# Kernel tuning notes

Measured on AMD Instinct MI355X. Metric: run time of the kernel, lower is better.

Reference implementation:

```python
import jax, jax.numpy as jnp
import numpy as np

N_NODES = 100000
N_EDGES = 1600000
N_GRAPHS = 64
IN_FEATS = 86  # 10 + |NodeTypes|(3) + |Devices|(5) + 2*2 + 2*32
GCN_H = 64
FC_H = 32
BN_EPS = 1e-5


def setup_inputs() -> dict:
    key = jax.random.key(0)
    ks = jax.random.split(key, 10)
    x = jax.random.normal(ks[0], (N_NODES, IN_FEATS), dtype=jnp.float32)
    edge_src = jax.random.randint(ks[1], (N_EDGES,), 0, N_NODES, dtype=jnp.int32)
    edge_dst = jax.random.randint(ks[2], (N_EDGES,), 0, N_NODES, dtype=jnp.int32)
    graph_ids = jnp.sort(jax.random.randint(ks[3], (N_NODES,), 0, N_GRAPHS, dtype=jnp.int32))
    bn_gamma = jnp.ones((IN_FEATS,), dtype=jnp.float32)
    bn_beta = jnp.zeros((IN_FEATS,), dtype=jnp.float32)
    W1 = jax.random.normal(ks[4], (IN_FEATS, GCN_H), dtype=jnp.float32) * 0.1
    b1 = jnp.zeros((GCN_H,), dtype=jnp.float32)
    W2 = jax.random.normal(ks[5], (GCN_H, GCN_H), dtype=jnp.float32) * 0.1
    b2 = jnp.zeros((GCN_H,), dtype=jnp.float32)
    fc1_w = jax.random.normal(ks[6], (GCN_H, FC_H), dtype=jnp.float32) * 0.1
    fc1_b = jnp.zeros((FC_H,), dtype=jnp.float32)
    fc2_w = jax.random.normal(ks[7], (FC_H, 1), dtype=jnp.float32) * 0.1
    fc2_b = jnp.zeros((1,), dtype=jnp.float32)
    return {"x": x, "edge_src": edge_src, "edge_dst": edge_dst,
            "graph_ids": graph_ids, "num_graphs": N_GRAPHS,
            "bn_gamma": bn_gamma, "bn_beta": bn_beta,
            "W1": W1, "b1": b1, "W2": W2, "b2": b2,
            "fc1_w": fc1_w, "fc1_b": fc1_b, "fc2_w": fc2_w, "fc2_b": fc2_b}


def _gcn_layer(h, edge_src, edge_dst, W, b):
    # DGL copy_src + mean reduce: each node's h is overwritten by the mean of
    # its in-neighbors' h; zero-in-degree nodes keep their old h (UDF reduce
    # is only applied to nodes with non-empty mailboxes).
    n = h.shape[0]
    msg_sum = jax.ops.segment_sum(h[edge_src], edge_dst, num_segments=n)  # [N, d]
    deg = jax.ops.segment_sum(jnp.ones_like(edge_dst, dtype=h.dtype), edge_dst, num_segments=n)
    agg = jnp.where(deg[:, None] > 0, msg_sum / jnp.maximum(deg, 1.0)[:, None], h)
    return jax.nn.relu(agg @ W + b)


def reference(x, edge_src, edge_dst, graph_ids, num_graphs,
              bn_gamma, bn_beta, W1, b1, W2, b2, fc1_w, fc1_b, fc2_w, fc2_b):
    # BatchNorm1d in training mode: batch stats, biased variance.
    mean = jnp.mean(x, axis=0)
    var = jnp.mean(jnp.square(x - mean), axis=0)
    h = (x - mean) * jax.lax.rsqrt(var + BN_EPS) * bn_gamma + bn_beta
    # Two GCN layers (mean message passing + linear + ReLU).
    h = _gcn_layer(h, edge_src, edge_dst, W1, b1)
    h = _gcn_layer(h, edge_src, edge_dst, W2, b2)
    # dgl.mean_nodes over the batched graph: per-graph mean of node features.
    g_sum = jax.ops.segment_sum(h, graph_ids, num_segments=num_graphs)  # [B, d]
    g_cnt = jax.ops.segment_sum(jnp.ones_like(graph_ids, dtype=h.dtype), graph_ids, num_segments=num_graphs)
    hg = g_sum / jnp.maximum(g_cnt, 1.0)[:, None]
    # FC head (no activation between the two linears, matching the source).
    hg = hg @ fc1_w + fc1_b
    hg = hg @ fc2_w + fc2_b
    return jax.nn.sigmoid(hg).squeeze()
```

## Files before the change

kernel.cpp:

```cpp
#include <hip/hip_runtime.h>

#define N_NODES 100000
#define N_EDGES 1600000
#define N_GRAPHS_C 64
#define IN_F 86
#define H 64
#define N_BKT 391
#define SC_EPT 8
#define SC_TILE 2048
#define SC_GRID 782
#define NW_POOL 2048
typedef unsigned short ushort;

__device__ inline float bf2f(ushort u) { return __uint_as_float(((unsigned)u) << 16); }
__device__ inline ushort f2bf(float f) {
    unsigned x = __float_as_uint(f);
    return (ushort)((x + 0x7fffu + ((x >> 16) & 1u)) >> 16);
}

__global__ void bn_stats_k(const float* __restrict__ x,
                           float* __restrict__ bnsum, float* __restrict__ bnsq) {
    __shared__ float s1[IN_F], s2[IN_F];
    int tid = threadIdx.x;
    if (tid < IN_F) { s1[tid] = 0.f; s2[tid] = 0.f; }
    __syncthreads();
    const int T = 430 * 256;
    int t = blockIdx.x * 256 + tid;
    float sum = 0.f, sq = 0.f;
    for (int idx = t; idx < N_NODES * IN_F; idx += T) {
        float v = x[idx];
        sum += v; sq += v * v;
    }
    int f = t % IN_F;
    atomicAdd(&s1[f], sum);
    atomicAdd(&s2[f], sq);
    __syncthreads();
    if (tid < IN_F) {
        atomicAdd(&bnsum[tid], s1[tid]);
        atomicAdd(&bnsq[tid], s2[tid]);
    }
}

__global__ void prep_k(const float* __restrict__ bnsum, const float* __restrict__ bnsq,
                       const float* __restrict__ gamma, const float* __restrict__ beta,
                       const float* __restrict__ W1, const float* __restrict__ b1,
                       float* __restrict__ W1p, float* __restrict__ c1) {
    __shared__ float scale[IN_F], shift[IN_F];
    int t = threadIdx.x;
    if (t < IN_F) {
        float mean = bnsum[t] * (1.0f / N_NODES);
        float var  = bnsq[t] * (1.0f / N_NODES) - mean * mean;
        float sc = gamma[t] * rsqrtf(var + 1e-5f);
        scale[t] = sc;
        shift[t] = beta[t] - mean * sc;
    }
    __syncthreads();
    for (int idx = t; idx < IN_F * H; idx += blockDim.x) {
        int i = idx / H;
        W1p[idx] = scale[i] * W1[idx];
    }
    if (t < H) {
        float acc = b1[t];
        for (int i = 0; i < IN_F; i++) acc += shift[i] * W1[i * H + t];
        c1[t] = acc;
    }
}

__global__ void bucket_count_k(const int* __restrict__ dst, int* __restrict__ bcnt) {
    __shared__ int hist[N_BKT];
    int tid = threadIdx.x;
    for (int i = tid; i < N_BKT; i += 256) hist[i] = 0;
    __syncthreads();
    int e0 = blockIdx.x * SC_TILE;
#pragma unroll
    for (int i = 0; i < SC_EPT; i++) {
        int e = e0 + i * 256 + tid;
        if (e < N_EDGES) atomicAdd(&hist[dst[e] >> 8], 1);
    }
    __syncthreads();
    for (int i = tid; i < N_BKT; i += 256) atomicAdd(&bcnt[i], hist[i]);
}

__global__ void bucket_scan_k(const int* __restrict__ bcnt, int* __restrict__ bstart,
                              int* __restrict__ gcursor) {
    __shared__ int tmp[512];
    int t = threadIdx.x;
    int v = (t < N_BKT) ? bcnt[t] : 0;
    tmp[t] = v;
    __syncthreads();
    for (int off = 1; off < 512; off <<= 1) {
        int a = (t >= off) ? tmp[t - off] : 0;
        __syncthreads();
        tmp[t] += a;
        __syncthreads();
    }
    if (t < N_BKT) { bstart[t] = tmp[t] - v; gcursor[t] = tmp[t] - v; }
    if (t == N_BKT - 1) bstart[N_BKT] = tmp[t];
}

__global__ void bucket_scatter_k(const int* __restrict__ src, const int* __restrict__ dst,
                                 int* __restrict__ gcursor, unsigned* __restrict__ ebkt) {
    __shared__ int hist[N_BKT];
    __shared__ int base[N_BKT];
    int tid = threadIdx.x;
    for (int i = tid; i < N_BKT; i += 256) hist[i] = 0;
    __syncthreads();
    int e0 = blockIdx.x * SC_TILE;
    unsigned pk[SC_EPT];
    int bk[SC_EPT], lo[SC_EPT];
#pragma unroll
    for (int i = 0; i < SC_EPT; i++) {
        int e = e0 + i * 256 + tid;
        if (e < N_EDGES) {
            int d = dst[e];
            pk[i] = ((unsigned)src[e] << 8) | (unsigned)(d & 255);
            bk[i] = d >> 8;
            lo[i] = atomicAdd(&hist[bk[i]], 1);
        }
    }
    __syncthreads();
    for (int i = tid; i < N_BKT; i += 256) base[i] = atomicAdd(&gcursor[i], hist[i]);
    __syncthreads();
#pragma unroll
    for (int i = 0; i < SC_EPT; i++) {
        int e = e0 + i * 256 + tid;
        if (e < N_EDGES) ebkt[base[bk[i]] + lo[i]] = pk[i];
    }
}

__global__ void bucket_fill_k(const unsigned* __restrict__ ebkt, const int* __restrict__ bstart,
                              int* __restrict__ rs, int* __restrict__ csr) {
    __shared__ int deg[256];
    __shared__ int scn[256];
    __shared__ int cur[256];
    int b = blockIdx.x;
    int tid = threadIdx.x;
    int e0 = bstart[b], e1 = bstart[b + 1];
    deg[tid] = 0;
    __syncthreads();
    for (int e = e0 + tid; e < e1; e += 256) atomicAdd(&deg[ebkt[e] & 255u], 1);
    __syncthreads();
    scn[tid] = deg[tid];
    __syncthreads();
    for (int off = 1; off < 256; off <<= 1) {
        int a = (tid >= off) ? scn[tid - off] : 0;
        __syncthreads();
        scn[tid] += a;
        __syncthreads();
    }
    int node = (b << 8) + tid;
    if (node < N_NODES) rs[node] = e0 + scn[tid];
    cur[tid] = e0 + scn[tid] - deg[tid];
    __syncthreads();
    for (int e = e0 + tid; e < e1; e += 256) {
        unsigned p = ebkt[e];
        int pos = atomicAdd(&cur[p & 255u], 1);
        csr[pos] = (int)(p >> 8);
    }
}

template <int K>
__global__ __launch_bounds__(256) void gemm_t(const float* __restrict__ X,
                                              const float* __restrict__ W,
                                              const float* __restrict__ bias,
                                              ushort* __restrict__ Y, int N) {
    __shared__ __align__(16) float Xl[64][K + 1];
    __shared__ __align__(16) float Wl[K][64];
    int tid = threadIdx.x;
    int row0 = blockIdx.x * 64;
    for (int i = tid; i < K * 64; i += 256) Wl[i / 64][i % 64] = W[i];
    for (int i = tid; i < 64 * K; i += 256) {
        int r = i / K, c = i % K;
        Xl[r][c] = (row0 + r < N) ? X[(size_t)(row0 + r) * K + c] : 0.f;
    }
    __syncthreads();
    int cg = tid & 15, rg = tid >> 4;
    float4 b4 = *(const float4*)&bias[cg * 4];
    float acc[4][4];
    for (int i = 0; i < 4; i++) { acc[i][0] = b4.x; acc[i][1] = b4.y; acc[i][2] = b4.z; acc[i][3] = b4.w; }
    for (int k = 0; k < K; k++) {
        float4 w = *(const float4*)&Wl[k][cg * 4];
        float x0 = Xl[rg * 4 + 0][k];
        float x1 = Xl[rg * 4 + 1][k];
        float x2 = Xl[rg * 4 + 2][k];
        float x3 = Xl[rg * 4 + 3][k];
        acc[0][0] += x0 * w.x; acc[0][1] += x0 * w.y; acc[0][2] += x0 * w.z; acc[0][3] += x0 * w.w;
        acc[1][0] += x1 * w.x; acc[1][1] += x1 * w.y; acc[1][2] += x1 * w.z; acc[1][3] += x1 * w.w;
        acc[2][0] += x2 * w.x; acc[2][1] += x2 * w.y; acc[2][2] += x2 * w.z; acc[2][3] += x2 * w.w;
        acc[3][0] += x3 * w.x; acc[3][1] += x3 * w.y; acc[3][2] += x3 * w.z; acc[3][3] += x3 * w.w;
    }
    for (int i = 0; i < 4; i++) {
        int gr = row0 + rg * 4 + i;
        if (gr < N) {
            ushort4 o;
            o.x = f2bf(acc[i][0]); o.y = f2bf(acc[i][1]);
            o.z = f2bf(acc[i][2]); o.w = f2bf(acc[i][3]);
            *(ushort4*)&Y[(size_t)gr * 64 + cg * 4] = o;
        }
    }
}

__global__ void gather_f32_k(const ushort* __restrict__ g, const int* __restrict__ rs,
                             const int* __restrict__ csr, float* __restrict__ out) {
    int lane = threadIdx.x & 63;
    int n = blockIdx.x * (blockDim.x >> 6) + (threadIdx.x >> 6);
    if (n >= N_NODES) return;
    int start = (n == 0) ? 0 : rs[n - 1];
    int end = rs[n];
    float a0 = 0.f, a1 = 0.f, a2 = 0.f, a3 = 0.f;
    for (int j0 = start; j0 < end; j0 += 64) {
        int cnt = min(64, end - j0);
        int myidx = (lane < cnt) ? csr[j0 + lane] : 0;
        int j = 0;
        for (; j + 3 < cnt; j += 4) {
            int s0 = __shfl(myidx, j, 64);
            int s1 = __shfl(myidx, j + 1, 64);
            int s2 = __shfl(myidx, j + 2, 64);
            int s3 = __shfl(myidx, j + 3, 64);
            a0 += bf2f(g[(size_t)s0 * H + lane]);
            a1 += bf2f(g[(size_t)s1 * H + lane]);
            a2 += bf2f(g[(size_t)s2 * H + lane]);
            a3 += bf2f(g[(size_t)s3 * H + lane]);
        }
        for (; j < cnt; j++) {
            int s = __shfl(myidx, j, 64);
            a0 += bf2f(g[(size_t)s * H + lane]);
        }
    }
    int d = end - start;
    float acc = (a0 + a1) + (a2 + a3);
    float val = (d > 0) ? acc / (float)d : bf2f(g[(size_t)n * H + lane]);
    out[(size_t)n * H + lane] = fmaxf(val, 0.f);
}

__global__ void gather_bf16_k(const ushort* __restrict__ g, const int* __restrict__ rs,
                              const int* __restrict__ csr, ushort* __restrict__ out) {
    int lane = threadIdx.x & 63;
    int n = blockIdx.x * (blockDim.x >> 6) + (threadIdx.x >> 6);
    if (n >= N_NODES) return;
    int start = (n == 0) ? 0 : rs[n - 1];
    int end = rs[n];
    float a0 = 0.f, a1 = 0.f, a2 = 0.f, a3 = 0.f;
    for (int j0 = start; j0 < end; j0 += 64) {
        int cnt = min(64, end - j0);
        int myidx = (lane < cnt) ? csr[j0 + lane] : 0;
        int j = 0;
        for (; j + 3 < cnt; j += 4) {
            int s0 = __shfl(myidx, j, 64);
            int s1 = __shfl(myidx, j + 1, 64);
            int s2 = __shfl(myidx, j + 2, 64);
            int s3 = __shfl(myidx, j + 3, 64);
            a0 += bf2f(g[(size_t)s0 * H + lane]);
            a1 += bf2f(g[(size_t)s1 * H + lane]);
            a2 += bf2f(g[(size_t)s2 * H + lane]);
            a3 += bf2f(g[(size_t)s3 * H + lane]);
        }
        for (; j < cnt; j++) {
            int s = __shfl(myidx, j, 64);
            a0 += bf2f(g[(size_t)s * H + lane]);
        }
    }
    int d = end - start;
    float acc = (a0 + a1) + (a2 + a3);
    float val = (d > 0) ? acc / (float)d : bf2f(g[(size_t)n * H + lane]);
    out[(size_t)n * H + lane] = f2bf(fmaxf(val, 0.f));
}

__global__ void pool_k(const ushort* __restrict__ h, const int* __restrict__ gid,
                       float* __restrict__ gsum, int* __restrict__ gcnt) {
    int lane = threadIdx.x & 63;
    int wpb = blockDim.x >> 6;
    int gw = blockIdx.x * wpb + (threadIdx.x >> 6);
    const int chunk = (N_NODES + NW_POOL - 1) / NW_POOL;
    int n0 = gw * chunk;
    if (n0 >= N_NODES) return;
    int n1 = min(n0 + chunk, N_NODES);
    float acc = 0.f;
    int cur = gid[n0], cnt = 0;
    for (int n = n0; n < n1; n++) {
        int g = gid[n];
        if (g != cur) {
            atomicAdd(&gsum[cur * H + lane], acc);
            if (lane == 0) atomicAdd(&gcnt[cur], cnt);
            cur = g; acc = 0.f; cnt = 0;
        }
        acc += bf2f(h[(size_t)n * H + lane]);
        cnt++;
    }
    atomicAdd(&gsum[cur * H + lane], acc);
    if (lane == 0) atomicAdd(&gcnt[cur], cnt);
}

__global__ void head_k(const float* __restrict__ gsum, const int* __restrict__ gcnt,
                       const float* __restrict__ fc1w, const float* __restrict__ fc1b,
                       const float* __restrict__ fc2w, const float* __restrict__ fc2b,
                       float* __restrict__ out) {
    __shared__ float w1[H * 32];
    __shared__ float w2[32], bb1[32];
    int b = threadIdx.x;
    for (int i = b; i < H * 32; i += 64) w1[i] = fc1w[i];
    if (b < 32) { w2[b] = fc2w[b]; bb1[b] = fc1b[b]; }
    __syncthreads();
    if (b >= N_GRAPHS_C) return;
    float hg[H];
    float inv = 1.0f / fmaxf((float)gcnt[b], 1.0f);
    for (int k = 0; k < H; k++) hg[k] = gsum[b * H + k] * inv;
    float z = fc2b[0];
    for (int j = 0; j < 32; j++) {
        float t = bb1[j];
        for (int k = 0; k < H; k++) t += hg[k] * w1[k * 32 + j];
        z += t * w2[j];
    }
    out[b] = 1.0f / (1.0f + expf(-z));
}

extern "C" void kernel_launch(void* const* d_in, const int* in_sizes, int n_in,
                              void* d_out, int out_size, void* d_ws, size_t ws_size,
                              hipStream_t stream) {
    const float* x        = (const float*)d_in[0];
    const int*   edge_src = (const int*)d_in[1];
    const int*   edge_dst = (const int*)d_in[2];
    const int*   gid      = (const int*)d_in[3];
    const float* bn_gamma = (const float*)d_in[5];
    const float* bn_beta  = (const float*)d_in[6];
    const float* W1       = (const float*)d_in[7];
    const float* b1       = (const float*)d_in[8];
    const float* W2       = (const float*)d_in[9];
    const float* b2       = (const float*)d_in[10];
    const float* fc1w     = (const float*)d_in[11];
    const float* fc1b     = (const float*)d_in[12];
    const float* fc2w     = (const float*)d_in[13];
    const float* fc2b     = (const float*)d_in[14];
    float* out = (float*)d_out;

    char* ws = (char*)d_ws;
    size_t off = 0;
    auto alloc = [&](size_t bytes) { void* p = ws + off; off += (bytes + 255) & ~(size_t)255; return p; };
    float* bnsum    = (float*)alloc(IN_F * sizeof(float) * 2);
    float* bnsq     = bnsum + IN_F;
    float* W1p      = (float*)alloc(IN_F * H * sizeof(float));
    float* c1       = (float*)alloc(H * sizeof(float));
    float* gsum     = (float*)alloc(N_GRAPHS_C * H * sizeof(float) + N_GRAPHS_C * sizeof(int));
    int*   gcnt     = (int*)(gsum + N_GRAPHS_C * H);
    int*   bcnt     = (int*)alloc(N_BKT * sizeof(int));
    int*   bstart   = (int*)alloc((N_BKT + 1) * sizeof(int));
    int*   gcursor  = (int*)alloc(N_BKT * sizeof(int));
    int*   rs       = (int*)alloc(N_NODES * sizeof(int));
    int*   csr      = (int*)alloc((size_t)N_EDGES * sizeof(int));
    ushort* gbuf    = (ushort*)alloc((size_t)N_NODES * H * sizeof(ushort));
    float* agg      = (float*)alloc((size_t)N_NODES * H * sizeof(float));
    unsigned* ebkt = (unsigned*)gbuf;
    ushort* h2 = (ushort*)agg;

    hipMemsetAsync(bnsum, 0, IN_F * sizeof(float) * 2, stream);
    hipMemsetAsync(bcnt, 0, N_BKT * sizeof(int), stream);
    hipMemsetAsync(gsum, 0, N_GRAPHS_C * H * sizeof(float) + N_GRAPHS_C * sizeof(int), stream);

    bucket_count_k<<<SC_GRID, 256, 0, stream>>>(edge_dst, bcnt);
    bucket_scan_k<<<1, 512, 0, stream>>>(bcnt, bstart, gcursor);
    bucket_scatter_k<<<SC_GRID, 256, 0, stream>>>(edge_src, edge_dst, gcursor, ebkt);
    bucket_fill_k<<<N_BKT, 256, 0, stream>>>(ebkt, bstart, rs, csr);

    bn_stats_k<<<430, 256, 0, stream>>>(x, bnsum, bnsq);
    prep_k<<<1, 256, 0, stream>>>(bnsum, bnsq, bn_gamma, bn_beta, W1, b1, W1p, c1);

    gemm_t<IN_F><<<(N_NODES + 63) / 64, 256, 0, stream>>>(x, W1p, c1, gbuf, N_NODES);
    gather_f32_k<<<(N_NODES + 3) / 4, 256, 0, stream>>>(gbuf, rs, csr, agg);

    gemm_t<H><<<(N_NODES + 63) / 64, 256, 0, stream>>>(agg, W2, b2, gbuf, N_NODES);
    gather_bf16_k<<<(N_NODES + 3) / 4, 256, 0, stream>>>(gbuf, rs, csr, h2);

    pool_k<<<NW_POOL / 4, 256, 0, stream>>>(h2, gid, gsum, gcnt);
    head_k<<<1, 64, 0, stream>>>(gsum, gcnt, fc1w, fc1b, fc2w, fc2b, out);
}
```

Baseline: 428.2 us.

## Fuse BN stats with bucket count, scan with prep, pool into gather; bf16 h1

Merges the BN statistics pass with the edge bucket histogram, and the bucket scan with the weight-prep kernel, which removes two launches. The layer-1 output is now stored as bf16 instead of fp32, with a bf16-input GEMM for layer 2, which halves that intermediate's traffic. The second gather now does graph pooling directly through per-node atomics. The gather inner loop is unrolled to 8 independent accumulators, and the three memsets are combined into one. Per-node atomics on 64 graph rows can cause heavy contention, and the bf16 intermediate adds rounding error.

New measurement: 1.079 ms. 2.52x slower.

```diff
diff --git a/kernel.cpp b/kernel.cpp
--- a/kernel.cpp
+++ b/kernel.cpp
@@ -9,7 +9,7 @@
 #define SC_EPT 8
 #define SC_TILE 2048
 #define SC_GRID 782
-#define NW_POOL 2048
+#define BC_GRID 860
 typedef unsigned short ushort;
 
 __device__ inline float bf2f(ushort u) { return __uint_as_float(((unsigned)u) << 16); }
@@ -18,13 +18,24 @@
     return (ushort)((x + 0x7fffu + ((x >> 16) & 1u)) >> 16);
 }
 
-__global__ void bn_stats_k(const float* __restrict__ x,
-                           float* __restrict__ bnsum, float* __restrict__ bnsq) {
+__global__ void bn_count_k(const float* __restrict__ x, const int* __restrict__ dst,
+                           float* __restrict__ bnsum, float* __restrict__ bnsq,
+                           int* __restrict__ bcnt) {
     __shared__ float s1[IN_F], s2[IN_F];
+    __shared__ int hist[N_BKT];
     int tid = threadIdx.x;
     if (tid < IN_F) { s1[tid] = 0.f; s2[tid] = 0.f; }
-    __syncthreads();
-    const int T = 430 * 256;
+    for (int i = tid; i < N_BKT; i += 256) hist[i] = 0;
+    __syncthreads();
+    if (blockIdx.x < SC_GRID) {
+        int e0 = blockIdx.x * SC_TILE;
+#pragma unroll
+        for (int i = 0; i < SC_EPT; i++) {
+            int e = e0 + i * 256 + tid;
+            if (e < N_EDGES) atomicAdd(&hist[dst[e] >> 8], 1);
+        }
+    }
+    const int T = BC_GRID * 256;
     int t = blockIdx.x * 256 + tid;
     float sum = 0.f, sq = 0.f;
     for (int idx = t; idx < N_NODES * IN_F; idx += T) {
@@ -39,14 +50,30 @@
         atomicAdd(&bnsum[tid], s1[tid]);
         atomicAdd(&bnsq[tid], s2[tid]);
     }
-}
-
-__global__ void prep_k(const float* __restrict__ bnsum, const float* __restrict__ bnsq,
-                       const float* __restrict__ gamma, const float* __restrict__ beta,
-                       const float* __restrict__ W1, const float* __restrict__ b1,
-                       float* __restrict__ W1p, float* __restrict__ c1) {
+    if (blockIdx.x < SC_GRID)
+        for (int i = tid; i < N_BKT; i += 256) atomicAdd(&bcnt[i], hist[i]);
+}
+
+__global__ void scanprep_k(const int* __restrict__ bcnt, int* __restrict__ bstart,
+                           int* __restrict__ gcursor,
+                           const float* __restrict__ bnsum, const float* __restrict__ bnsq,
+                           const float* __restrict__ gamma, const float* __restrict__ beta,
+                           const float* __restrict__ W1, const float* __restrict__ b1,
+                           float* __restrict__ W1p, float* __restrict__ c1) {
+    __shared__ int tmp[512];
     __shared__ float scale[IN_F], shift[IN_F];
     int t = threadIdx.x;
+    int v = (t < N_BKT) ? bcnt[t] : 0;
+    tmp[t] = v;
+    __syncthreads();
+    for (int off = 1; off < 512; off <<= 1) {
+        int a = (t >= off) ? tmp[t - off] : 0;
+        __syncthreads();
+        tmp[t] += a;
+        __syncthreads();
+    }
+    if (t < N_BKT) { bstart[t] = tmp[t] - v; gcursor[t] = tmp[t] - v; }
+    if (t == N_BKT - 1) bstart[N_BKT] = tmp[t];
     if (t < IN_F) {
         float mean = bnsum[t] * (1.0f / N_NODES);
         float var  = bnsq[t] * (1.0f / N_NODES) - mean * mean;
@@ -55,47 +82,12 @@
         shift[t] = beta[t] - mean * sc;
     }
     __syncthreads();
-    for (int idx = t; idx < IN_F * H; idx += blockDim.x) {
-        int i = idx / H;
-        W1p[idx] = scale[i] * W1[idx];
-    }
+    for (int idx = t; idx < IN_F * H; idx += 512) W1p[idx] = scale[idx / H] * W1[idx];
     if (t < H) {
         float acc = b1[t];
         for (int i = 0; i < IN_F; i++) acc += shift[i] * W1[i * H + t];
         c1[t] = acc;
     }
-}
-
-__global__ void bucket_count_k(const int* __restrict__ dst, int* __restrict__ bcnt) {
-    __shared__ int hist[N_BKT];
-    int tid = threadIdx.x;
-    for (int i = tid; i < N_BKT; i += 256) hist[i] = 0;
-    __syncthreads();
-    int e0 = blockIdx.x * SC_TILE;
-#pragma unroll
-    for (int i = 0; i < SC_EPT; i++) {
-        int e = e0 + i * 256 + tid;
-        if (e < N_EDGES) atomicAdd(&hist[dst[e] >> 8], 1);
-    }
-    __syncthreads();
-    for (int i = tid; i < N_BKT; i += 256) atomicAdd(&bcnt[i], hist[i]);
-}
-
-__global__ void bucket_scan_k(const int* __restrict__ bcnt, int* __restrict__ bstart,
-                              int* __restrict__ gcursor) {
-    __shared__ int tmp[512];
-    int t = threadIdx.x;
-    int v = (t < N_BKT) ? bcnt[t] : 0;
-    tmp[t] = v;
-    __syncthreads();
-    for (int off = 1; off < 512; off <<= 1) {
-        int a = (t >= off) ? tmp[t - off] : 0;
-        __syncthreads();
-        tmp[t] += a;
-        __syncthreads();
-    }
-    if (t < N_BKT) { bstart[t] = tmp[t] - v; gcursor[t] = tmp[t] - v; }
-    if (t == N_BKT - 1) bstart[N_BKT] = tmp[t];
 }
 
 __global__ void bucket_scatter_k(const int* __restrict__ src, const int* __restrict__ dst,
@@ -159,13 +151,13 @@
     }
 }
 
-template <int K>
-__global__ __launch_bounds__(256) void gemm_t(const float* __restrict__ X,
-                                              const float* __restrict__ W,
-                                              const float* __restrict__ bias,
-                                              ushort* __restrict__ Y, int N) {
-    __shared__ __align__(16) float Xl[64][K + 1];
-    __shared__ __align__(16) float Wl[K][64];
+__global__ __launch_bounds__(256) void gemm_f32_k(const float* __restrict__ X,
+                                                  const float* __restrict__ W,
+                                                  const float* __restrict__ bias,
+                                                  ushort* __restrict__ Y, int N) {
+    const int K = IN_F;
+    __shared__ __align__(16) float Xl[64][IN_F + 1];
+    __shared__ __align__(16) float Wl[IN_F][64];
     int tid = threadIdx.x;
     int row0 = blockIdx.x * 64;
     for (int i = tid; i < K * 64; i += 256) Wl[i / 64][i % 64] = W[i];
@@ -200,18 +192,80 @@
     }
 }
 
-__global__ void gather_f32_k(const ushort* __restrict__ g, const int* __restrict__ rs,
-                             const int* __restrict__ csr, float* __restrict__ out) {
-    int lane = threadIdx.x & 63;
-    int n = blockIdx.x * (blockDim.x >> 6) + (threadIdx.x >> 6);
-    if (n >= N_NODES) return;
-    int start = (n == 0) ? 0 : rs[n - 1];
-    int end = rs[n];
+__global__ __launch_bounds__(256) void gemm_bf16_k(const ushort* __restrict__ X,
+                                                   const float* __restrict__ W,
+                                                   const float* __restrict__ bias,
+                                                   ushort* __restrict__ Y, int N) {
+    const int K = H;
+    __shared__ __align__(16) float Xl[64][H + 1];
+    __shared__ __align__(16) float Wl[H][64];
+    int tid = threadIdx.x;
+    int row0 = blockIdx.x * 64;
+    for (int i = tid; i < K * 64; i += 256) Wl[i / 64][i % 64] = W[i];
+    for (int i = tid; i < 64 * 16; i += 256) {
+        int r = i >> 4, c4 = (i & 15) * 4;
+        if (row0 + r < N) {
+            ushort4 u = *(const ushort4*)&X[(size_t)(row0 + r) * K + c4];
+            Xl[r][c4 + 0] = bf2f(u.x); Xl[r][c4 + 1] = bf2f(u.y);
+            Xl[r][c4 + 2] = bf2f(u.z); Xl[r][c4 + 3] = bf2f(u.w);
+        } else {
+            Xl[r][c4 + 0] = 0.f; Xl[r][c4 + 1] = 0.f;
+            Xl[r][c4 + 2] = 0.f; Xl[r][c4 + 3] = 0.f;
+        }
+    }
+    __syncthreads();
+    int cg = tid & 15, rg = tid >> 4;
+    float4 b4 = *(const float4*)&bias[cg * 4];
+    float acc[4][4];
+    for (int i = 0; i < 4; i++) { acc[i][0] = b4.x; acc[i][1] = b4.y; acc[i][2] = b4.z; acc[i][3] = b4.w; }
+    for (int k = 0; k < K; k++) {
+        float4 w = *(const float4*)&Wl[k][cg * 4];
+        float x0 = Xl[rg * 4 + 0][k];
+        float x1 = Xl[rg * 4 + 1][k];
+        float x2 = Xl[rg * 4 + 2][k];
+        float x3 = Xl[rg * 4 + 3][k];
+        acc[0][0] += x0 * w.x; acc[0][1] += x0 * w.y; acc[0][2] += x0 * w.z; acc[0][3] += x0 * w.w;
+        acc[1][0] += x1 * w.x; acc[1][1] += x1 * w.y; acc[1][2] += x1 * w.z; acc[1][3] += x1 * w.w;
+        acc[2][0] += x2 * w.x; acc[2][1] += x2 * w.y; acc[2][2] += x2 * w.z; acc[2][3] += x2 * w.w;
+        acc[3][0] += x3 * w.x; acc[3][1] += x3 * w.y; acc[3][2] += x3 * w.z; acc[3][3] += x3 * w.w;
+    }
+    for (int i = 0; i < 4; i++) {
+        int gr = row0 + rg * 4 + i;
+        if (gr < N) {
+            ushort4 o;
+            o.x = f2bf(acc[i][0]); o.y = f2bf(acc[i][1]);
+            o.z = f2bf(acc[i][2]); o.w = f2bf(acc[i][3]);
+            *(ushort4*)&Y[(size_t)gr * 64 + cg * 4] = o;
+        }
+    }
+}
+
+__device__ inline float gather_row(const ushort* __restrict__ g, const int* __restrict__ csr,
+                                   int start, int end, int lane) {
     float a0 = 0.f, a1 = 0.f, a2 = 0.f, a3 = 0.f;
+    float a4 = 0.f, a5 = 0.f, a6 = 0.f, a7 = 0.f;
     for (int j0 = start; j0 < end; j0 += 64) {
         int cnt = min(64, end - j0);
         int myidx = (lane < cnt) ? csr[j0 + lane] : 0;
         int j = 0;
+        for (; j + 7 < cnt; j += 8) {
+            int s0 = __shfl(myidx, j, 64);
+            int s1 = __shfl(myidx, j + 1, 64);
+            int s2 = __shfl(myidx, j + 2, 64);
+            int s3 = __shfl(myidx, j + 3, 64);
+            int s4 = __shfl(myidx, j + 4, 64);
+            int s5 = __shfl(myidx, j + 5, 64);
+            int s6 = __shfl(myidx, j + 6, 64);
+            int s7 = __shfl(myidx, j + 7, 64);
+            a0 += bf2f(g[(size_t)s0 * H + lane]);
+            a1 += bf2f(g[(size_t)s1 * H + lane]);
+            a2 += bf2f(g[(size_t)s2 * H + lane]);
+            a3 += bf2f(g[(size_t)s3 * H + lane]);
+            a4 += bf2f(g[(size_t)s4 * H + lane]);
+            a5 += bf2f(g[(size_t)s5 * H + lane]);
+            a6 += bf2f(g[(size_t)s6 * H + lane]);
+            a7 += bf2f(g[(size_t)s7 * H + lane]);
+        }
         for (; j + 3 < cnt; j += 4) {
             int s0 = __shfl(myidx, j, 64);
             int s1 = __shfl(myidx, j + 1, 64);
@@ -227,68 +281,37 @@
             a0 += bf2f(g[(size_t)s * H + lane]);
         }
     }
-    int d = end - start;
-    float acc = (a0 + a1) + (a2 + a3);
-    float val = (d > 0) ? acc / (float)d : bf2f(g[(size_t)n * H + lane]);
-    out[(size_t)n * H + lane] = fmaxf(val, 0.f);
-}
-
-__global__ void gather_bf16_k(const ushort* __restrict__ g, const int* __restrict__ rs,
-                              const int* __restrict__ csr, ushort* __restrict__ out) {
+    return ((a0 + a1) + (a2 + a3)) + ((a4 + a5) + (a6 + a7));
+}
+
+__global__ void gather1_k(const ushort* __restrict__ g, const int* __restrict__ rs,
+                          const int* __restrict__ csr, ushort* __restrict__ out) {
     int lane = threadIdx.x & 63;
-    int n = blockIdx.x * (blockDim.x >> 6) + (threadIdx.x >> 6);
+    int n = blockIdx.x * 4 + (threadIdx.x >> 6);
     if (n >= N_NODES) return;
     int start = (n == 0) ? 0 : rs[n - 1];
     int end = rs[n];
-    float a0 = 0.f, a1 = 0.f, a2 = 0.f, a3 = 0.f;
-    for (int j0 = start; j0 < end; j0 += 64) {
-        int cnt = min(64, end - j0);
-        int myidx = (lane < cnt) ? csr[j0 + lane] : 0;
-        int j = 0;
-        for (; j + 3 < cnt; j += 4) {
-            int s0 = __shfl(myidx, j, 64);
-            int s1 = __shfl(myidx, j + 1, 64);
-            int s2 = __shfl(myidx, j + 2, 64);
-            int s3 = __shfl(myidx, j + 3, 64);
-            a0 += bf2f(g[(size_t)s0 * H + lane]);
-            a1 += bf2f(g[(size_t)s1 * H + lane]);
-            a2 += bf2f(g[(size_t)s2 * H + lane]);
-            a3 += bf2f(g[(size_t)s3 * H + lane]);
-        }
-        for (; j < cnt; j++) {
-            int s = __shfl(myidx, j, 64);
-            a0 += bf2f(g[(size_t)s * H + lane]);
-        }
-    }
+    float acc = gather_row(g, csr, start, end, lane);
     int d = end - start;
-    float acc = (a0 + a1) + (a2 + a3);
     float val = (d > 0) ? acc / (float)d : bf2f(g[(size_t)n * H + lane]);
     out[(size_t)n * H + lane] = f2bf(fmaxf(val, 0.f));
 }
 
-__global__ void pool_k(const ushort* __restrict__ h, const int* __restrict__ gid,
-                       float* __restrict__ gsum, int* __restrict__ gcnt) {
+__global__ void gather2_pool_k(const ushort* __restrict__ g, const int* __restrict__ rs,
+                               const int* __restrict__ csr, const int* __restrict__ gid,
+                               float* __restrict__ gsum, int* __restrict__ gcnt) {
     int lane = threadIdx.x & 63;
-    int wpb = blockDim.x >> 6;
-    int gw = blockIdx.x * wpb + (threadIdx.x >> 6);
-    const int chunk = (N_NODES + NW_POOL - 1) / NW_POOL;
-    int n0 = gw * chunk;
-    if (n0 >= N_NODES) return;
-    int n1 = min(n0 + chunk, N_NODES);
-    float acc = 0.f;
-    int cur = gid[n0], cnt = 0;
-    for (int n = n0; n < n1; n++) {
-        int g = gid[n];
-        if (g != cur) {
-            atomicAdd(&gsum[cur * H + lane], acc);
-            if (lane == 0) atomicAdd(&gcnt[cur], cnt);
-            cur = g; acc = 0.f; cnt = 0;
-        }
-        acc += bf2f(h[(size_t)n * H + lane]);
-        cnt++;
-    }
-    atomicAdd(&gsum[cur * H + lane], acc);
-    if (lane == 0) atomicAdd(&gcnt[cur], cnt);
+    int n = blockIdx.x * 4 + (threadIdx.x >> 6);
+    if (n >= N_NODES) return;
+    int start = (n == 0) ? 0 : rs[n - 1];
+    int end = rs[n];
+    float acc = gather_row(g, csr, start, end, lane);
+    int d = end - start;
+    float val = (d > 0) ? acc / (float)d : bf2f(g[(size_t)n * H + lane]);
+    val = fmaxf(val, 0.f);
+    int gg = gid[n];
+    atomicAdd(&gsum[gg * H + lane], val);
+    if (lane == 0) atomicAdd(&gcnt[gg], 1);
 }
 
 __global__ void head_k(const float* __restrict__ gsum, const int* __restrict__ gcnt,
@@ -336,40 +359,36 @@
     char* ws = (char*)d_ws;
     size_t off = 0;
     auto alloc = [&](size_t bytes) { void* p = ws + off; off += (bytes + 255) & ~(size_t)255; return p; };
-    float* bnsum    = (float*)alloc(IN_F * sizeof(float) * 2);
-    float* bnsq     = bnsum + IN_F;
-    float* W1p      = (float*)alloc(IN_F * H * sizeof(float));
-    float* c1       = (float*)alloc(H * sizeof(float));
-    float* gsum     = (float*)alloc(N_GRAPHS_C * H * sizeof(float) + N_GRAPHS_C * sizeof(int));
-    int*   gcnt     = (int*)(gsum + N_GRAPHS_C * H);
-    int*   bcnt     = (int*)alloc(N_BKT * sizeof(int));
-    int*   bstart   = (int*)alloc((N_BKT + 1) * sizeof(int));
-    int*   gcursor  = (int*)alloc(N_BKT * sizeof(int));
-    int*   rs       = (int*)alloc(N_NODES * sizeof(int));
-    int*   csr      = (int*)alloc((size_t)N_EDGES * sizeof(int));
-    ushort* gbuf    = (ushort*)alloc((size_t)N_NODES * H * sizeof(ushort));
-    float* agg      = (float*)alloc((size_t)N_NODES * H * sizeof(float));
+    const size_t ZW = IN_F + IN_F + N_BKT + N_GRAPHS_C * H + N_GRAPHS_C;
+    float* zreg  = (float*)alloc(ZW * sizeof(float));
+    float* bnsum = zreg;
+    float* bnsq  = bnsum + IN_F;
+    int*   bcnt  = (int*)(bnsq + IN_F);
+    float* gsum  = (float*)(bcnt + N_BKT);
+    int*   gcnt  = (int*)(gsum + N_GRAPHS_C * H);
+    float* W1p     = (float*)alloc(IN_F * H * sizeof(float));
+    float* c1      = (float*)alloc(H * sizeof(float));
+    int*   bstart  = (int*)alloc((N_BKT + 1) * sizeof(int));
+    int*   gcursor = (int*)alloc(N_BKT * sizeof(int));
+    int*   rs      = (int*)alloc(N_NODES * sizeof(int));
+    int*   csr     = (int*)alloc((size_t)N_EDGES * sizeof(int));
+    ushort* gbuf   = (ushort*)alloc((size_t)N_NODES * H * sizeof(ushort));
+    ushort* h1     = (ushort*)alloc((size_t)N_NODES * H * sizeof(ushort));
     unsigned* ebkt = (unsigned*)gbuf;
-    ushort* h2 = (ushort*)agg;
-
-    hipMemsetAsync(bnsum, 0, IN_F * sizeof(float) * 2, stream);
-    hipMemsetAsync(bcnt, 0, N_BKT * sizeof(int), stream);
-    hipMemsetAsync(gsum, 0, N_GRAPHS_C * H * sizeof(float) + N_GRAPHS_C * sizeof(int), stream);
-
-    bucket_count_k<<<SC_GRID, 256, 0, stream>>>(edge_dst, bcnt);
-    bucket_scan_k<<<1, 512, 0, stream>>>(bcnt, bstart, gcursor);
+
+    hipMemsetAsync(zreg, 0, ZW * sizeof(float), stream);
+
+    bn_count_k<<<BC_GRID, 256, 0, stream>>>(x, edge_dst, bnsum, bnsq, bcnt);
+    scanprep_k<<<1, 512, 0, stream>>>(bcnt, bstart, gcursor, bnsum, bnsq,
+                                      bn_gamma, bn_beta, W1, b1, W1p, c1);
     bucket_scatter_k<<<SC_GRID, 256, 0, stream>>>(edge_src, edge_dst, gcursor, ebkt);
     bucket_fill_k<<<N_BKT, 256, 0, stream>>>(ebkt, bstart, rs, csr);
 
-    bn_stats_k<<<430, 256, 0, stream>>>(x, bnsum, bnsq);
-    prep_k<<<1, 256, 0, stream>>>(bnsum, bnsq, bn_gamma, bn_beta, W1, b1, W1p, c1);
-
-    gemm_t<IN_F><<<(N_NODES + 63) / 64, 256, 0, stream>>>(x, W1p, c1, gbuf, N_NODES);
-    gather_f32_k<<<(N_NODES + 3) / 4, 256, 0, stream>>>(gbuf, rs, csr, agg);
-
-    gemm_t<H><<<(N_NODES + 63) / 64, 256, 0, stream>>>(agg, W2, b2, gbuf, N_NODES);
-    gather_bf16_k<<<(N_NODES + 3) / 4, 256, 0, stream>>>(gbuf, rs, csr, h2);
-
-    pool_k<<<NW_POOL / 4, 256, 0, stream>>>(h2, gid, gsum, gcnt);
+    gemm_f32_k<<<(N_NODES + 63) / 64, 256, 0, stream>>>(x, W1p, c1, gbuf, N_NODES);
+    gather1_k<<<(N_NODES + 3) / 4, 256, 0, stream>>>(gbuf, rs, csr, h1);
+
+    gemm_bf16_k<<<(N_NODES + 63) / 64, 256, 0, stream>>>(h1, W2, b2, gbuf, N_NODES);
+    gather2_pool_k<<<(N_NODES + 3) / 4, 256, 0, stream>>>(gbuf, rs, csr, gid, gsum, gcnt);
+
     head_k<<<1, 64, 0, stream>>>(gsum, gcnt, fc1w, fc1b, fc2w, fc2b, out);
 }
```
